# Kernel tuning notes

Measured on AMD Instinct MI355X. Metric: run time of the kernel, lower is better.

Reference implementation:

```python
import jax, jax.numpy as jnp
import numpy as np

VAR_CENTER = 0.1   # variances[0]
VAR_SIZE = 0.2     # variances[1]
IOU_THRESHOLD = 0.5

B, T, P = 16, 64, 100000


def setup_inputs() -> dict:
    key = jax.random.key(0)
    kpc, kps, kc, ks, kl = jax.random.split(key, 5)
    # Priors in (cx, cy, w, h), relative coords in [0,1]
    p_cxcy = jax.random.uniform(kpc, (P, 2), dtype=jnp.float32) * 0.9 + 0.05
    p_wh = jax.random.uniform(kps, (P, 2), dtype=jnp.float32) * 0.15 + 0.02
    priors_xywha = jnp.concatenate([p_cxcy, p_wh], axis=-1)
    # Ground-truth boxes in xyxy (valid: x2>x1, y2>y1)
    centers = jax.random.uniform(kc, (B, T, 2), dtype=jnp.float32) * 0.8 + 0.1
    sizes = jax.random.uniform(ks, (B, T, 2), dtype=jnp.float32) * 0.15 + 0.02
    gt_boxes = jnp.concatenate([centers - sizes / 2, centers + sizes / 2], axis=-1)
    gt_labels = jax.random.randint(kl, (B, T), 1, 81, dtype=jnp.int32)
    return {"priors_xywha": priors_xywha, "gt_boxes": gt_boxes, "gt_labels": gt_labels}


def _box_iou(boxes1, boxes2):
    # boxes1: [T,4] xyxy, boxes2: [P,4] xyxy -> [T,P]
    area1 = (boxes1[:, 2] - boxes1[:, 0]) * (boxes1[:, 3] - boxes1[:, 1])  # [T]
    area2 = (boxes2[:, 2] - boxes2[:, 0]) * (boxes2[:, 3] - boxes2[:, 1])  # [P]
    lt = jnp.maximum(boxes1[:, None, :2], boxes2[None, :, :2])  # [T,P,2]
    rb = jnp.minimum(boxes1[:, None, 2:], boxes2[None, :, 2:])  # [T,P,2]
    wh = jnp.clip(rb - lt, 0.0)
    inter = wh[..., 0] * wh[..., 1]  # [T,P]
    return inter / (area1[:, None] + area2[None, :] - inter)


def reference(priors_xywha, gt_boxes, gt_labels):
    p_cxcy = priors_xywha[:, :2]
    p_wh = priors_xywha[:, 2:]
    priors_xyxy = jnp.concatenate([p_cxcy - p_wh / 2, p_cxcy + p_wh / 2], axis=-1)

    def per_image(boxes, labels):
        # boxes [T,4], labels [T]
        iou = _box_iou(boxes, priors_xyxy)            # [T,P]
        matched_vals = jnp.max(iou, axis=0)           # [P] best IoU per prior
        matches = jnp.argmax(iou, axis=0)             # [P] target index per prior
        best_prior = jnp.argmax(iou, axis=1)          # [T] best prior per target
        matches = matches.at[best_prior].set(jnp.arange(T))
        matched_vals = matched_vals.at[best_prior].set(2.0)
        lbl = labels[matches]                         # [P] irregular gather
        lbl = jnp.where(matched_vals < IOU_THRESHOLD, 0, lbl)
        mboxes = boxes[matches]                       # [P,4]
        b_cxcy = (mboxes[:, :2] + mboxes[:, 2:]) / 2
        b_wh = mboxes[:, 2:] - mboxes[:, :2]
        g_cxcy = (b_cxcy - p_cxcy) / (VAR_CENTER * p_wh)
        g_wh = jnp.log(b_wh / p_wh) / VAR_SIZE
        loc = jnp.concatenate([g_cxcy, g_wh], axis=-1)  # [P,4]
        return loc, lbl

    gt_locations, out_labels = jax.vmap(per_image)(gt_boxes, gt_labels)
    return gt_locations, out_labels
```

## Files before the change

kernel.cpp:

```cpp
#include <hip/hip_runtime.h>

#define T_GT 64
#define KP 4
#define TPB 256
#define NB 64

typedef unsigned int u32;
typedef unsigned long long u64;

__global__ void __launch_bounds__(256)
match_main(const float4* __restrict__ priors,
           const float4* __restrict__ gt_boxes,
           const int* __restrict__ gt_labels,
           u64* __restrict__ part,
           float* __restrict__ out_loc,
           float* __restrict__ out_lbl,
           int P, int NG) {
    __shared__ float s_gx0[T_GT], s_gy0[T_GT], s_gx1[T_GT], s_gy1[T_GT];
    __shared__ int   s_lbl[T_GT];
    __shared__ u64   s_best[4][T_GT];
    __shared__ u64   s_tab[4][NB];

    const int tid  = threadIdx.x;
    const int lane = tid & 63;
    const int wv   = tid >> 6;
    const int b    = blockIdx.y;
    const int pbase = blockIdx.x * (TPB * KP);

    const float4 gb = gt_boxes[b * T_GT + lane];

    if (wv == 0) {
        s_gx0[lane] = gb.x;
        s_gy0[lane] = gb.y;
        s_gx1[lane] = gb.z;
        s_gy1[lane] = gb.w;
        s_lbl[lane] = gt_labels[b * T_GT + lane];
    }
    s_best[wv][lane] = (u64)0xFFFFFFFFu;

    if (wv == 0) {
        #pragma unroll 8
        for (int bin = 0; bin < NB; ++bin) {
            const u64 m = __ballot(gb.z > (float)bin * (1.0f / NB));
            if (lane == 0) s_tab[0][bin] = m;
        }
    } else if (wv == 1) {
        #pragma unroll 8
        for (int bin = 0; bin < NB; ++bin) {
            const u64 m = __ballot(gb.x < (float)(bin + 1) * (1.0f / NB));
            if (lane == 0) s_tab[1][bin] = m;
        }
    } else if (wv == 2) {
        #pragma unroll 8
        for (int bin = 0; bin < NB; ++bin) {
            const u64 m = __ballot(gb.w > (float)bin * (1.0f / NB));
            if (lane == 0) s_tab[2][bin] = m;
        }
    } else {
        #pragma unroll 8
        for (int bin = 0; bin < NB; ++bin) {
            const u64 m = __ballot(gb.y < (float)(bin + 1) * (1.0f / NB));
            if (lane == 0) s_tab[3][bin] = m;
        }
    }
    __syncthreads();

    #pragma unroll
    for (int k = 0; k < KP; ++k) {
        const int p = pbase + k * TPB + tid;
        if (p < P) {
            const float4 pr = priors[p];
            const float px0 = __fsub_rn(pr.x, __fmul_rn(0.5f, pr.z));
            const float py0 = __fsub_rn(pr.y, __fmul_rn(0.5f, pr.w));
            const float px1 = __fadd_rn(pr.x, __fmul_rn(0.5f, pr.z));
            const float py1 = __fadd_rn(pr.y, __fmul_rn(0.5f, pr.w));
            const float pa  = __fmul_rn(__fsub_rn(px1, px0),
                                        __fsub_rn(py1, py0));

            const int bx0 = min(max(__float2int_rd(px0 * (float)NB), 0), NB - 1);
            const int bx1 = min(max(__float2int_rd(px1 * (float)NB), 0), NB - 1);
            const int by0 = min(max(__float2int_rd(py0 * (float)NB), 0), NB - 1);
            const int by1 = min(max(__float2int_rd(py1 * (float)NB), 0), NB - 1);

            u64 mask = s_tab[0][bx0] & s_tab[1][bx1] &
                       s_tab[2][by0] & s_tab[3][by1];

            u64 mbest = 63u;
            while (mask) {
                const int t = (int)__builtin_ctzll(mask);
                mask &= mask - 1;
                const float gx0 = s_gx0[t];
                const float gy0 = s_gy0[t];
                const float gx1 = s_gx1[t];
                const float gy1 = s_gy1[t];
                const float gar = __fmul_rn(__fsub_rn(gx1, gx0),
                                            __fsub_rn(gy1, gy0));

                const float wx = fmaxf(__fsub_rn(fminf(gx1, px1),
                                                 fmaxf(gx0, px0)), 0.0f);
                const float wy = fmaxf(__fsub_rn(fminf(gy1, py1),
                                                 fmaxf(gy0, py0)), 0.0f);
                const float inter = __fmul_rn(wx, wy);
                if (inter > 0.0f) {
                    const float uni = __fsub_rn(__fadd_rn(gar, pa), inter);
                    const float q = __fdiv_rn(inter, uni);
                    const u64 qh = (u64)__float_as_uint(q) << 32;
                    const u64 mp = qh | (u32)(63 - t);
                    if (mp > mbest) mbest = mp;
                    atomicMax(&s_best[wv][t],
                              qh | (u64)(0xFFFFFFFFu - (u32)p));
                }
            }

            const int   t_best = 63 - (int)(mbest & 63u);
            const float q_best = __uint_as_float((u32)(mbest >> 32));
            const int   lbl = (q_best < 0.5f) ? 0 : s_lbl[t_best];

            const float mx0 = s_gx0[t_best];
            const float my0 = s_gy0[t_best];
            const float mx1 = s_gx1[t_best];
            const float my1 = s_gy1[t_best];

            const float bcx = (mx0 + mx1) * 0.5f;
            const float bcy = (my0 + my1) * 0.5f;
            const float bw  = mx1 - mx0;
            const float bh  = my1 - my0;

            const float lx = __fdividef(bcx - pr.x, 0.1f * pr.z);
            const float ly = __fdividef(bcy - pr.y, 0.1f * pr.w);
            const float lz = __logf(__fdividef(bw, pr.z)) * 5.0f;
            const float lw = __logf(__fdividef(bh, pr.w)) * 5.0f;

            float4* rowp = (float4*)(out_loc + ((size_t)b * P + p) * 4);
            *rowp = make_float4(lx, ly, lz, lw);
            out_lbl[(size_t)b * P + p] = (float)lbl;
        }
    }

    __syncthreads();
    if (tid < T_GT) {
        u64 m = s_best[0][tid];
        #pragma unroll
        for (int w = 1; w < 4; ++w) {
            const u64 v = s_best[w][tid];
            if (v > m) m = v;
        }
        part[((size_t)b * NG + blockIdx.x) * T_GT + tid] = m;
    }
}

__global__ void __launch_bounds__(256)
match_fin(const float4* __restrict__ priors,
          const float4* __restrict__ gt_boxes,
          const int* __restrict__ gt_labels,
          const u64* __restrict__ part,
          float* __restrict__ out_loc,
          float* __restrict__ out_lbl,
          int P, int NG) {
    __shared__ float4 s_gt[T_GT];
    __shared__ int    s_lbl[T_GT];
    __shared__ u64    s_best[4][T_GT];
    __shared__ u32    s_p[T_GT];

    const int tid = threadIdx.x;
    const int b   = blockIdx.x;
    const int t   = tid & 63;
    const int w   = tid >> 6;

    if (tid < T_GT) {
        s_gt[tid]  = gt_boxes[b * T_GT + tid];
        s_lbl[tid] = gt_labels[b * T_GT + tid];
    }

    const size_t base = (size_t)b * NG * T_GT + t;
    u64 m = 0;
    int g = w;
    for (; g + 12 < NG; g += 16) {
        const u64 a0 = part[base + (size_t)g * T_GT];
        const u64 a1 = part[base + (size_t)(g + 4) * T_GT];
        const u64 a2 = part[base + (size_t)(g + 8) * T_GT];
        const u64 a3 = part[base + (size_t)(g + 12) * T_GT];
        u64 x = a0 > a1 ? a0 : a1;
        const u64 y = a2 > a3 ? a2 : a3;
        if (y > x) x = y;
        if (x > m) m = x;
    }
    for (; g < NG; g += 4) {
        const u64 v = part[base + (size_t)g * T_GT];
        if (v > m) m = v;
    }
    s_best[w][t] = m;
    __syncthreads();
    if (tid < T_GT) {
        m = s_best[0][t];
        #pragma unroll
        for (int i = 1; i < 4; ++i) {
            const u64 v = s_best[i][t];
            if (v > m) m = v;
        }
        s_p[t] = 0xFFFFFFFFu - (u32)(m & 0xFFFFFFFFull);
    }
    __syncthreads();
    if (tid >= T_GT) return;

    const u32 p = s_p[tid];
    for (int u = tid + 1; u < T_GT; ++u)
        if (s_p[u] == p) return;

    const float4 pr = priors[p];
    const float4 mb = s_gt[tid];
    const float  bcx = (mb.x + mb.z) * 0.5f;
    const float  bcy = (mb.y + mb.w) * 0.5f;
    const float  bw  = mb.z - mb.x;
    const float  bh  = mb.w - mb.y;

    const float lx = __fdividef(bcx - pr.x, 0.1f * pr.z);
    const float ly = __fdividef(bcy - pr.y, 0.1f * pr.w);
    const float lz = __logf(__fdividef(bw, pr.z)) * 5.0f;
    const float lw = __logf(__fdividef(bh, pr.w)) * 5.0f;

    float4* rowp = (float4*)(out_loc + ((size_t)b * P + p) * 4);
    *rowp = make_float4(lx, ly, lz, lw);
    out_lbl[(size_t)b * P + p] = (float)s_lbl[tid];
}

extern "C" void kernel_launch(void* const* d_in, const int* in_sizes, int n_in,
                              void* d_out, int out_size, void* d_ws, size_t ws_size,
                              hipStream_t stream) {
    const float4* priors    = (const float4*)d_in[0];
    const float4* gt_boxes  = (const float4*)d_in[1];
    const int*    gt_labels = (const int*)d_in[2];

    const int P = in_sizes[0] / 4;
    const int B = in_sizes[2] / T_GT;

    float* out_loc = (float*)d_out;
    float* out_lbl = out_loc + (size_t)B * P * 4;

    const int NG = (P + TPB * KP - 1) / (TPB * KP);
    u64* part = (u64*)d_ws;

    dim3 g(NG, B);
    match_main<<<g, TPB, 0, stream>>>(priors, gt_boxes, gt_labels, part,
                                      out_loc, out_lbl, P, NG);
    match_fin<<<dim3(B), TPB, 0, stream>>>(priors, gt_boxes, gt_labels, part,
                                           out_loc, out_lbl, P, NG);
}
```

Measured before the change: 105.3 us.

## Prefetch priors before barrier, software-pipeline candidate loop with float4 GT loads

Moves the prior loads for all KP iterations ahead of the table-building barrier, clamping the index so every lane loads. Stores GT boxes as float4 in shared memory and software-pipelines the candidate loop so the next candidate's box is read while the current IoU is computed. The `inter > 0` branch is removed, so every candidate does the divide and atomicMax, and out-of-range lanes do full work with clamped indices. This targets load latency and LDS instruction count but adds divides and shared atomics for candidates that do not overlap.

```diff
diff --git a/kernel.cpp b/kernel.cpp
--- a/kernel.cpp
+++ b/kernel.cpp
@@ -16,10 +16,10 @@
            float* __restrict__ out_loc,
            float* __restrict__ out_lbl,
            int P, int NG) {
-    __shared__ float s_gx0[T_GT], s_gy0[T_GT], s_gx1[T_GT], s_gy1[T_GT];
-    __shared__ int   s_lbl[T_GT];
-    __shared__ u64   s_best[4][T_GT];
-    __shared__ u64   s_tab[4][NB];
+    __shared__ float4 s_gt[T_GT];
+    __shared__ int    s_lbl[T_GT];
+    __shared__ u64    s_best[4][T_GT];
+    __shared__ u64    s_tab[4][NB];
 
     const int tid  = threadIdx.x;
     const int lane = tid & 63;
@@ -30,10 +30,7 @@
     const float4 gb = gt_boxes[b * T_GT + lane];
 
     if (wv == 0) {
-        s_gx0[lane] = gb.x;
-        s_gy0[lane] = gb.y;
-        s_gx1[lane] = gb.z;
-        s_gy1[lane] = gb.w;
+        s_gt[lane]  = gb;
         s_lbl[lane] = gt_labels[b * T_GT + lane];
     }
     s_best[wv][lane] = (u64)0xFFFFFFFFu;
@@ -63,74 +60,80 @@
             if (lane == 0) s_tab[3][bin] = m;
         }
     }
+
+    float4 prk[KP];
+    #pragma unroll
+    for (int k = 0; k < KP; ++k)
+        prk[k] = priors[min(pbase + k * TPB + tid, P - 1)];
+
     __syncthreads();
 
     #pragma unroll
     for (int k = 0; k < KP; ++k) {
-        const int p = pbase + k * TPB + tid;
+        const int p  = pbase + k * TPB + tid;
+        const float4 pr = prk[k];
+        const float px0 = __fsub_rn(pr.x, __fmul_rn(0.5f, pr.z));
+        const float py0 = __fsub_rn(pr.y, __fmul_rn(0.5f, pr.w));
+        const float px1 = __fadd_rn(pr.x, __fmul_rn(0.5f, pr.z));
+        const float py1 = __fadd_rn(pr.y, __fmul_rn(0.5f, pr.w));
+        const float pa  = __fmul_rn(__fsub_rn(px1, px0),
+                                    __fsub_rn(py1, py0));
+
+        const int bx0 = min(max(__float2int_rd(px0 * (float)NB), 0), NB - 1);
+        const int bx1 = min(max(__float2int_rd(px1 * (float)NB), 0), NB - 1);
+        const int by0 = min(max(__float2int_rd(py0 * (float)NB), 0), NB - 1);
+        const int by1 = min(max(__float2int_rd(py1 * (float)NB), 0), NB - 1);
+
+        u64 mask = s_tab[0][bx0] & s_tab[1][bx1] &
+                   s_tab[2][by0] & s_tab[3][by1];
+
+        u64 mbest = 63u;
+
+        bool live = (mask != 0);
+        int  t0 = live ? (int)__builtin_ctzll(mask) : 0;
+        mask &= mask - 1;
+        float4 g0 = s_gt[t0];
+
+        while (live) {
+            const bool live1 = (mask != 0);
+            const int  t1 = live1 ? (int)__builtin_ctzll(mask) : 0;
+            mask &= mask - 1;
+            const float4 g1 = s_gt[t1];
+
+            const float gar = __fmul_rn(__fsub_rn(g0.z, g0.x),
+                                        __fsub_rn(g0.w, g0.y));
+            const float wx = fmaxf(__fsub_rn(fminf(g0.z, px1),
+                                             fmaxf(g0.x, px0)), 0.0f);
+            const float wy = fmaxf(__fsub_rn(fminf(g0.w, py1),
+                                             fmaxf(g0.y, py0)), 0.0f);
+            const float inter = __fmul_rn(wx, wy);
+            const float uni = __fsub_rn(__fadd_rn(gar, pa), inter);
+            const float q = __fdiv_rn(inter, uni);
+            const u64 qh = (u64)__float_as_uint(q) << 32;
+            const u64 mp = qh | (u32)(63 - t0);
+            if (mp > mbest) mbest = mp;
+            atomicMax(&s_best[wv][t0],
+                      qh | (u64)(0xFFFFFFFFu - (u32)min(p, P - 1)));
+
+            g0 = g1; t0 = t1; live = live1;
+        }
+
+        const int   t_best = 63 - (int)(mbest & 63u);
+        const float q_best = __uint_as_float((u32)(mbest >> 32));
+        const int   lbl = (q_best < 0.5f) ? 0 : s_lbl[t_best];
+
+        const float4 mb = s_gt[t_best];
+        const float bcx = (mb.x + mb.z) * 0.5f;
+        const float bcy = (mb.y + mb.w) * 0.5f;
+        const float bw  = mb.z - mb.x;
+        const float bh  = mb.w - mb.y;
+
+        const float lx = __fdividef(bcx - pr.x, 0.1f * pr.z);
+        const float ly = __fdividef(bcy - pr.y, 0.1f * pr.w);
+        const float lz = __logf(__fdividef(bw, pr.z)) * 5.0f;
+        const float lw = __logf(__fdividef(bh, pr.w)) * 5.0f;
+
         if (p < P) {
-            const float4 pr = priors[p];
-            const float px0 = __fsub_rn(pr.x, __fmul_rn(0.5f, pr.z));
-            const float py0 = __fsub_rn(pr.y, __fmul_rn(0.5f, pr.w));
-            const float px1 = __fadd_rn(pr.x, __fmul_rn(0.5f, pr.z));
-            const float py1 = __fadd_rn(pr.y, __fmul_rn(0.5f, pr.w));
-            const float pa  = __fmul_rn(__fsub_rn(px1, px0),
-                                        __fsub_rn(py1, py0));
-
-            const int bx0 = min(max(__float2int_rd(px0 * (float)NB), 0), NB - 1);
-            const int bx1 = min(max(__float2int_rd(px1 * (float)NB), 0), NB - 1);
-            const int by0 = min(max(__float2int_rd(py0 * (float)NB), 0), NB - 1);
-            const int by1 = min(max(__float2int_rd(py1 * (float)NB), 0), NB - 1);
-
-            u64 mask = s_tab[0][bx0] & s_tab[1][bx1] &
-                       s_tab[2][by0] & s_tab[3][by1];
-
-            u64 mbest = 63u;
-            while (mask) {
-                const int t = (int)__builtin_ctzll(mask);
-                mask &= mask - 1;
-                const float gx0 = s_gx0[t];
-                const float gy0 = s_gy0[t];
-                const float gx1 = s_gx1[t];
-                const float gy1 = s_gy1[t];
-                const float gar = __fmul_rn(__fsub_rn(gx1, gx0),
-                                            __fsub_rn(gy1, gy0));
-
-                const float wx = fmaxf(__fsub_rn(fminf(gx1, px1),
-                                                 fmaxf(gx0, px0)), 0.0f);
-                const float wy = fmaxf(__fsub_rn(fminf(gy1, py1),
-                                                 fmaxf(gy0, py0)), 0.0f);
-                const float inter = __fmul_rn(wx, wy);
-                if (inter > 0.0f) {
-                    const float uni = __fsub_rn(__fadd_rn(gar, pa), inter);
-                    const float q = __fdiv_rn(inter, uni);
-                    const u64 qh = (u64)__float_as_uint(q) << 32;
-                    const u64 mp = qh | (u32)(63 - t);
-                    if (mp > mbest) mbest = mp;
-                    atomicMax(&s_best[wv][t],
-                              qh | (u64)(0xFFFFFFFFu - (u32)p));
-                }
-            }
-
-            const int   t_best = 63 - (int)(mbest & 63u);
-            const float q_best = __uint_as_float((u32)(mbest >> 32));
-            const int   lbl = (q_best < 0.5f) ? 0 : s_lbl[t_best];
-
-            const float mx0 = s_gx0[t_best];
-            const float my0 = s_gy0[t_best];
-            const float mx1 = s_gx1[t_best];
-            const float my1 = s_gy1[t_best];
-
-            const float bcx = (mx0 + mx1) * 0.5f;
-            const float bcy = (my0 + my1) * 0.5f;
-            const float bw  = mx1 - mx0;
-            const float bh  = my1 - my0;
-
-            const float lx = __fdividef(bcx - pr.x, 0.1f * pr.z);
-            const float ly = __fdividef(bcy - pr.y, 0.1f * pr.w);
-            const float lz = __logf(__fdividef(bw, pr.z)) * 5.0f;
-            const float lw = __logf(__fdividef(bh, pr.w)) * 5.0f;
-
             float4* rowp = (float4*)(out_loc + ((size_t)b * P + p) * 4);
             *rowp = make_float4(lx, ly, lz, lw);
             out_lbl[(size_t)b * P + p] = (float)lbl;
```

Measured after the change: 104.1 us. About the same (-1.1%).

## Compact per-wave candidate pairs in LDS to balance IoU work across lanes

Applied to the files above, without the earlier changes.

Each wave builds a compacted list of (prior, target) candidate pairs in shared memory using a wave-wide prefix sum. All 64 lanes then evaluate the pairs uniformly, instead of each lane looping over its own variable-length mask, which removes divergence from uneven candidate counts. Per-prior bests are merged with shared-memory atomicMax, and any overflow beyond the capacity is handled by the old per-lane loop. All prior loads are also hoisted ahead of the sync. The cost is added LDS usage, a prefix-scan per prior batch, and extra atomics.

```diff
diff --git a/kernel.cpp b/kernel.cpp
--- a/kernel.cpp
+++ b/kernel.cpp
@@ -4,6 +4,7 @@
 #define KP 4
 #define TPB 256
 #define NB 64
+#define CAP 768
 
 typedef unsigned int u32;
 typedef unsigned long long u64;
@@ -20,6 +21,10 @@
     __shared__ int   s_lbl[T_GT];
     __shared__ u64   s_best[4][T_GT];
     __shared__ u64   s_tab[4][NB];
+    __shared__ float s_px0[4][64], s_py0[4][64], s_px1[4][64], s_py1[4][64];
+    __shared__ u32   s_pp[4][64];
+    __shared__ u64   s_pbest[4][64];
+    __shared__ unsigned short s_cand[4][CAP];
 
     const int tid  = threadIdx.x;
     const int lane = tid & 63;
@@ -63,74 +68,141 @@
             if (lane == 0) s_tab[3][bin] = m;
         }
     }
+
+    float4 prk[KP];
+    #pragma unroll
+    for (int k = 0; k < KP; ++k)
+        prk[k] = priors[min(pbase + k * TPB + tid, P - 1)];
+
     __syncthreads();
 
     #pragma unroll
     for (int k = 0; k < KP; ++k) {
-        const int p = pbase + k * TPB + tid;
+        const int p  = pbase + k * TPB + tid;
+        const int pe = min(p, P - 1);
+        const float4 pr = prk[k];
+        const float px0 = __fsub_rn(pr.x, __fmul_rn(0.5f, pr.z));
+        const float py0 = __fsub_rn(pr.y, __fmul_rn(0.5f, pr.w));
+        const float px1 = __fadd_rn(pr.x, __fmul_rn(0.5f, pr.z));
+        const float py1 = __fadd_rn(pr.y, __fmul_rn(0.5f, pr.w));
+        const float pa  = __fmul_rn(__fsub_rn(px1, px0),
+                                    __fsub_rn(py1, py0));
+
+        const int bx0 = min(max(__float2int_rd(px0 * (float)NB), 0), NB - 1);
+        const int bx1 = min(max(__float2int_rd(px1 * (float)NB), 0), NB - 1);
+        const int by0 = min(max(__float2int_rd(py0 * (float)NB), 0), NB - 1);
+        const int by1 = min(max(__float2int_rd(py1 * (float)NB), 0), NB - 1);
+
+        const u64 mask = s_tab[0][bx0] & s_tab[1][bx1] &
+                         s_tab[2][by0] & s_tab[3][by1];
+
+        s_px0[wv][lane] = px0;
+        s_py0[wv][lane] = py0;
+        s_px1[wv][lane] = px1;
+        s_py1[wv][lane] = py1;
+        s_pp [wv][lane] = (u32)pe;
+        s_pbest[wv][lane] = 63u;
+
+        const int cnt = (int)__builtin_popcountll(mask);
+        int inc = cnt;
+        #pragma unroll
+        for (int d = 1; d < 64; d <<= 1) {
+            const int v = __shfl_up(inc, d, 64);
+            if (lane >= d) inc += v;
+        }
+        const int excl = inc - cnt;
+        const int C    = __shfl(inc, 63, 64);
+
+        u64 mrem = mask;
+        int off  = excl;
+        while (mrem && off < CAP) {
+            const int t = (int)__builtin_ctzll(mrem);
+            mrem &= mrem - 1;
+            s_cand[wv][off++] = (unsigned short)((lane << 6) | t);
+        }
+
+        const int Cc = (C < CAP) ? C : CAP;
+        const int iters = (Cc + 63) >> 6;
+        int j   = lane;
+        u32 rec = (j < Cc) ? (u32)s_cand[wv][j] : 0u;
+        for (int it = 0; it < iters; ++it) {
+            const bool act = (j < Cc);
+            const int  jn  = j + 64;
+            const u32  recn = (jn < Cc) ? (u32)s_cand[wv][jn] : 0u;
+            const int o = (int)(rec >> 6) & 63;
+            const int t = (int)(rec & 63u);
+            const float gx0 = s_gx0[t], gy0 = s_gy0[t];
+            const float gx1 = s_gx1[t], gy1 = s_gy1[t];
+            const float qx0 = s_px0[wv][o], qy0 = s_py0[wv][o];
+            const float qx1 = s_px1[wv][o], qy1 = s_py1[wv][o];
+            const u32   po  = s_pp[wv][o];
+            const float qa  = __fmul_rn(__fsub_rn(qx1, qx0),
+                                        __fsub_rn(qy1, qy0));
+            const float gar = __fmul_rn(__fsub_rn(gx1, gx0),
+                                        __fsub_rn(gy1, gy0));
+            const float wx = fmaxf(__fsub_rn(fminf(gx1, qx1),
+                                             fmaxf(gx0, qx0)), 0.0f);
+            const float wy = fmaxf(__fsub_rn(fminf(gy1, qy1),
+                                             fmaxf(gy0, qy0)), 0.0f);
+            const float inter = __fmul_rn(wx, wy);
+            if (act && inter > 0.0f) {
+                const float uni = __fsub_rn(__fadd_rn(gar, qa), inter);
+                const float q = __fdiv_rn(inter, uni);
+                const u64 qh = (u64)__float_as_uint(q) << 32;
+                atomicMax(&s_best[wv][t], qh | (u64)(0xFFFFFFFFu - po));
+                atomicMax(&s_pbest[wv][o], qh | (u64)(u32)(63 - t));
+            }
+            rec = recn; j = jn;
+        }
+
+        u64 mbest = 63u;
+        while (mrem) {
+            const int t = (int)__builtin_ctzll(mrem);
+            mrem &= mrem - 1;
+            const float gx0 = s_gx0[t], gy0 = s_gy0[t];
+            const float gx1 = s_gx1[t], gy1 = s_gy1[t];
+            const float gar = __fmul_rn(__fsub_rn(gx1, gx0),
+                                        __fsub_rn(gy1, gy0));
+            const float wx = fmaxf(__fsub_rn(fminf(gx1, px1),
+                                             fmaxf(gx0, px0)), 0.0f);
+            const float wy = fmaxf(__fsub_rn(fminf(gy1, py1),
+                                             fmaxf(gy0, py0)), 0.0f);
+            const float inter = __fmul_rn(wx, wy);
+            if (inter > 0.0f) {
+                const float uni = __fsub_rn(__fadd_rn(gar, pa), inter);
+                const float q = __fdiv_rn(inter, uni);
+                const u64 qh = (u64)__float_as_uint(q) << 32;
+                const u64 mp = qh | (u32)(63 - t);
+                if (mp > mbest) mbest = mp;
+                atomicMax(&s_best[wv][t], qh | (u64)(0xFFFFFFFFu - (u32)pe));
+            }
+        }
+
+        {
+            const u64 v = s_pbest[wv][lane];
+            if (v > mbest) mbest = v;
+        }
+
+        const int   t_best = 63 - (int)(mbest & 63u);
+        const float q_best = __uint_as_float((u32)(mbest >> 32));
+        const int   lbl = (q_best < 0.5f) ? 0 : s_lbl[t_best];
+
+        const float mx0 = s_gx0[t_best];
+        const float my0 = s_gy0[t_best];
+        const float mx1 = s_gx1[t_best];
+        const float my1 = s_gy1[t_best];
+
+        const float bcx = (mx0 + mx1) * 0.5f;
+        const float bcy = (my0 + my1) * 0.5f;
+        const float bw  = mx1 - mx0;
+        const float bh  = my1 - my0;
+
+        const float lx = __fdividef(bcx - pr.x, 0.1f * pr.z);
+        const float ly = __fdividef(bcy - pr.y, 0.1f * pr.w);
+        const float lz = __logf(__fdividef(bw, pr.z)) * 5.0f;
+        const float lw = __logf(__fdividef(bh, pr.w)) * 5.0f;
+
         if (p < P) {
-            const float4 pr = priors[p];
-            const float px0 = __fsub_rn(pr.x, __fmul_rn(0.5f, pr.z));
-            const float py0 = __fsub_rn(pr.y, __fmul_rn(0.5f, pr.w));
-            const float px1 = __fadd_rn(pr.x, __fmul_rn(0.5f, pr.z));
-            const float py1 = __fadd_rn(pr.y, __fmul_rn(0.5f, pr.w));
-            const float pa  = __fmul_rn(__fsub_rn(px1, px0),
-                                        __fsub_rn(py1, py0));
-
-            const int bx0 = min(max(__float2int_rd(px0 * (float)NB), 0), NB - 1);
-            const int bx1 = min(max(__float2int_rd(px1 * (float)NB), 0), NB - 1);
-            const int by0 = min(max(__float2int_rd(py0 * (float)NB), 0), NB - 1);
-            const int by1 = min(max(__float2int_rd(py1 * (float)NB), 0), NB - 1);
-
-            u64 mask = s_tab[0][bx0] & s_tab[1][bx1] &
-                       s_tab[2][by0] & s_tab[3][by1];
-
-            u64 mbest = 63u;
-            while (mask) {
-                const int t = (int)__builtin_ctzll(mask);
-                mask &= mask - 1;
-                const float gx0 = s_gx0[t];
-                const float gy0 = s_gy0[t];
-                const float gx1 = s_gx1[t];
-                const float gy1 = s_gy1[t];
-                const float gar = __fmul_rn(__fsub_rn(gx1, gx0),
-                                            __fsub_rn(gy1, gy0));
-
-                const float wx = fmaxf(__fsub_rn(fminf(gx1, px1),
-                                                 fmaxf(gx0, px0)), 0.0f);
-                const float wy = fmaxf(__fsub_rn(fminf(gy1, py1),
-                                                 fmaxf(gy0, py0)), 0.0f);
-                const float inter = __fmul_rn(wx, wy);
-                if (inter > 0.0f) {
-                    const float uni = __fsub_rn(__fadd_rn(gar, pa), inter);
-                    const float q = __fdiv_rn(inter, uni);
-                    const u64 qh = (u64)__float_as_uint(q) << 32;
-                    const u64 mp = qh | (u32)(63 - t);
-                    if (mp > mbest) mbest = mp;
-                    atomicMax(&s_best[wv][t],
-                              qh | (u64)(0xFFFFFFFFu - (u32)p));
-                }
-            }
-
-            const int   t_best = 63 - (int)(mbest & 63u);
-            const float q_best = __uint_as_float((u32)(mbest >> 32));
-            const int   lbl = (q_best < 0.5f) ? 0 : s_lbl[t_best];
-
-            const float mx0 = s_gx0[t_best];
-            const float my0 = s_gy0[t_best];
-            const float mx1 = s_gx1[t_best];
-            const float my1 = s_gy1[t_best];
-
-            const float bcx = (mx0 + mx1) * 0.5f;
-            const float bcy = (my0 + my1) * 0.5f;
-            const float bw  = mx1 - mx0;
-            const float bh  = my1 - my0;
-
-            const float lx = __fdividef(bcx - pr.x, 0.1f * pr.z);
-            const float ly = __fdividef(bcy - pr.y, 0.1f * pr.w);
-            const float lz = __logf(__fdividef(bw, pr.z)) * 5.0f;
-            const float lw = __logf(__fdividef(bh, pr.w)) * 5.0f;
-
             float4* rowp = (float4*)(out_loc + ((size_t)b * P + p) * 4);
             *rowp = make_float4(lx, ly, lz, lw);
             out_lbl[(size_t)b * P + p] = (float)lbl;
```

Measured after the change: 106.6 us. No clear change (+1.2%).
